# Optimization experiments

Hardware: AMD Instinct MI355X
Metric: run time of the kernel (lower is better)

The kernel has to match this reference:

```python
import jax, jax.numpy as jnp
import numpy as np

N_NODES = 100000
N_EDGES = 1600000
IN_CH = 128


def _sage_conv(x, src, dst, Wl, b, Wr, n_nodes):
    # PyG SAGEConv (aggr='mean', root_weight=True):
    #   out_i = lin_l(mean_{j->i} x_j) + lin_r(x_i)
    msg = x[src]                                             # [E, F]
    agg = jax.ops.segment_sum(msg, dst, num_segments=n_nodes)  # [N, F]
    deg = jax.ops.segment_sum(jnp.ones((src.shape[0],), x.dtype), dst,
                              num_segments=n_nodes)          # [N]
    mean = agg / jnp.maximum(deg, 1.0)[:, None]
    return mean @ Wl + b + x @ Wr


def setup_inputs() -> dict:
    key = jax.random.key(0)
    ks = jax.random.split(key, 10)
    x = jax.random.normal(ks[0], (N_NODES, IN_CH), dtype=jnp.float32)
    edge_index = jax.random.randint(ks[1], (2, N_EDGES), 0, N_NODES, dtype=jnp.int64)
    s = 0.05
    return {
        "x": x,
        "edge_index": edge_index,
        "W1l": jax.random.normal(ks[2], (IN_CH, 32), dtype=jnp.float32) * s,
        "b1": jax.random.normal(ks[3], (32,), dtype=jnp.float32) * s,
        "W1r": jax.random.normal(ks[4], (IN_CH, 32), dtype=jnp.float32) * s,
        "W2l": jax.random.normal(ks[5], (32, 16), dtype=jnp.float32) * s,
        "b2": jax.random.normal(ks[6], (16,), dtype=jnp.float32) * s,
        "W2r": jax.random.normal(ks[7], (32, 16), dtype=jnp.float32) * s,
        "Wfc": jax.random.normal(ks[8], (16, 2), dtype=jnp.float32) * s,
        "bfc": jax.random.normal(ks[9], (2,), dtype=jnp.float32) * s,
    }


def reference(x, edge_index, W1l, b1, W1r, W2l, b2, W2r, Wfc, bfc):
    src, dst = edge_index[0], edge_index[1]
    n = x.shape[0]
    h = jax.nn.relu(_sage_conv(x, src, dst, W1l, b1, W1r, n))   # [N, 32]
    h = jax.nn.relu(_sage_conv(h, src, dst, W2l, b2, W2r, n))   # [N, 16]
    return h @ Wfc + bfc                                        # [N, 2]
```

## Files before the change

kernel.cpp:

```cpp
#include <hip/hip_runtime.h>

#define TPB 256
#define BK_SHIFT 7
#define BK_SIZE 128
#define NBK_MAX 784
#define CAP 2816
#define SC_EPB 8192
#define GEMM_BLKS 1024

typedef __attribute__((ext_vector_type(8))) short bf16x8;
typedef __attribute__((ext_vector_type(4))) float f32x4;
typedef __attribute__((ext_vector_type(2))) float f32x2;
typedef __attribute__((ext_vector_type(4))) unsigned short u16x4;

__device__ __forceinline__ unsigned short f2bf(float f) {
    unsigned u = __float_as_uint(f);
    unsigned r = (u + 0x7FFFu + ((u >> 16) & 1u)) >> 16;
    return (unsigned short)r;
}
__device__ __forceinline__ float bf2f(unsigned short b) {
    return __uint_as_float((unsigned)b << 16);
}
__device__ __forceinline__ void acc4(f32x4& a, u16x4 v) {
    a.x += bf2f(v.x); a.y += bf2f(v.y); a.z += bf2f(v.z); a.w += bf2f(v.w);
}

__global__ __launch_bounds__(256) void build_and_gemm1(
    const int* __restrict__ src, const int* __restrict__ dst,
    int* __restrict__ gfill, int* __restrict__ pk, int E, int NBK, int NSC,
    const float* __restrict__ A,
    const float* __restrict__ Wl,
    const float* __restrict__ Wr,
    const float* __restrict__ b,
    unsigned short* __restrict__ Yb,
    float* __restrict__ C,
    int N)
{
    __shared__ int lcnt[NBK_MAX];
    __shared__ int lbase[NBK_MAX];
    __shared__ int lrank[NBK_MAX];

    if ((int)blockIdx.x < NSC) {
        const int t = threadIdx.x;
        const int e0 = blockIdx.x * SC_EPB;

        for (int i = t; i < NBK; i += 256) { lcnt[i] = 0; lrank[i] = 0; }
        __syncthreads();

        #pragma unroll
        for (int k = 0; k < SC_EPB / 1024; ++k) {
            int e = e0 + k * 1024 + t * 4;
            if (e < E) {
                int4 d = *(const int4*)&dst[e];
                atomicAdd(&lcnt[d.x >> BK_SHIFT], 1);
                atomicAdd(&lcnt[d.y >> BK_SHIFT], 1);
                atomicAdd(&lcnt[d.z >> BK_SHIFT], 1);
                atomicAdd(&lcnt[d.w >> BK_SHIFT], 1);
            }
        }
        __syncthreads();

        for (int i = t; i < NBK; i += 256) {
            int c = lcnt[i];
            if (c) lbase[i] = atomicAdd(&gfill[i], c);
        }
        __syncthreads();

        #pragma unroll
        for (int k = 0; k < SC_EPB / 1024; ++k) {
            int e = e0 + k * 1024 + t * 4;
            if (e < E) {
                int4 d = *(const int4*)&dst[e];
                int4 s = *(const int4*)&src[e];
                {
                    int bb = d.x >> BK_SHIFT;
                    int pos = lbase[bb] + atomicAdd(&lrank[bb], 1);
                    if (pos < CAP) pk[(size_t)bb * CAP + pos] =
                        (s.x << BK_SHIFT) | (d.x & (BK_SIZE - 1));
                }
                {
                    int bb = d.y >> BK_SHIFT;
                    int pos = lbase[bb] + atomicAdd(&lrank[bb], 1);
                    if (pos < CAP) pk[(size_t)bb * CAP + pos] =
                        (s.y << BK_SHIFT) | (d.y & (BK_SIZE - 1));
                }
                {
                    int bb = d.z >> BK_SHIFT;
                    int pos = lbase[bb] + atomicAdd(&lrank[bb], 1);
                    if (pos < CAP) pk[(size_t)bb * CAP + pos] =
                        (s.z << BK_SHIFT) | (d.z & (BK_SIZE - 1));
                }
                {
                    int bb = d.w >> BK_SHIFT;
                    int pos = lbase[bb] + atomicAdd(&lrank[bb], 1);
                    if (pos < CAP) pk[(size_t)bb * CAP + pos] =
                        (s.w << BK_SHIFT) | (d.w & (BK_SIZE - 1));
                }
            }
        }
        return;
    }

    const int lane = threadIdx.x & 63;
    const int m    = lane & 15;
    const int quad = lane >> 4;
    const int wave   = (blockIdx.x - NSC) * (blockDim.x >> 6) + (threadIdx.x >> 6);
    const int nwaves = GEMM_BLKS * (blockDim.x >> 6);
    const int ntiles = (N + 15) >> 4;

    bf16x8 Bf[4][4];
    #pragma unroll
    for (int kc = 0; kc < 4; ++kc) {
        #pragma unroll
        for (int jt = 0; jt < 4; ++jt) {
            const float* W = (jt < 2) ? Wl : Wr;
            const int col = (jt & 1) * 16 + m;
            #pragma unroll
            for (int j = 0; j < 8; ++j) {
                int k = kc * 32 + quad * 8 + j;
                Bf[kc][jt][j] = (short)f2bf(W[k * 32 + col]);
            }
        }
    }

    const float bias0 = b[m];
    const float bias1 = b[16 + m];

    for (int tile = wave; tile < ntiles; tile += nwaves) {
        const int node0 = tile * 16;
        const int gn = node0 + m;
        const bool okA = gn < N;
        const float* rowp = A + (size_t)gn * 128;

        bf16x8 Af[4];
        #pragma unroll
        for (int kc = 0; kc < 4; ++kc) {
            f32x4 v0 = {0.f, 0.f, 0.f, 0.f};
            f32x4 v1 = {0.f, 0.f, 0.f, 0.f};
            if (okA) {
                v0 = __builtin_nontemporal_load((const f32x4*)&rowp[kc * 32 + quad * 8]);
                v1 = __builtin_nontemporal_load((const f32x4*)&rowp[kc * 32 + quad * 8 + 4]);
            }
            Af[kc][0] = (short)f2bf(v0.x); Af[kc][1] = (short)f2bf(v0.y);
            Af[kc][2] = (short)f2bf(v0.z); Af[kc][3] = (short)f2bf(v0.w);
            Af[kc][4] = (short)f2bf(v1.x); Af[kc][5] = (short)f2bf(v1.y);
            Af[kc][6] = (short)f2bf(v1.z); Af[kc][7] = (short)f2bf(v1.w);
        }

        f32x4 acc[4] = {{0.f,0.f,0.f,0.f},{0.f,0.f,0.f,0.f},
                        {0.f,0.f,0.f,0.f},{0.f,0.f,0.f,0.f}};
        #pragma unroll
        for (int kc = 0; kc < 4; ++kc) {
            #pragma unroll
            for (int jt = 0; jt < 4; ++jt)
                acc[jt] = __builtin_amdgcn_mfma_f32_16x16x32_bf16(
                    Af[kc], Bf[kc][jt], acc[jt], 0, 0, 0);
        }

        const int nodeBase = node0 + quad * 4;
        #pragma unroll
        for (int reg = 0; reg < 4; ++reg) {
            const int node = nodeBase + reg;
            if (node < N) {
                Yb[(size_t)node * 32 + m]      = f2bf(acc[0][reg]);
                Yb[(size_t)node * 32 + 16 + m] = f2bf(acc[1][reg]);
                C [(size_t)node * 32 + m]      = acc[2][reg] + bias0;
                C [(size_t)node * 32 + 16 + m] = acc[3][reg] + bias1;
            }
        }
    }
}

__global__ __launch_bounds__(256) void gather_gemm2(
    const int* __restrict__ gfill, const int* __restrict__ pk,
    const unsigned short* __restrict__ Yb,
    const float* __restrict__ c1,
    const float* __restrict__ W2l, const float* __restrict__ W2r,
    const float* __restrict__ b2,
    unsigned short* __restrict__ y2b, float* __restrict__ c2, int N)
{
    __shared__ int lcnt[BK_SIZE];
    __shared__ int soff[BK_SIZE];
    __shared__ int wcur[BK_SIZE];
    __shared__ int sidx[CAP];

    const int t = threadIdx.x;
    const int b = blockIdx.x;
    const size_t base = (size_t)b * CAP;
    const int cnt  = min(gfill[b], CAP);
    const int node0 = b * BK_SIZE;

    if (t < BK_SIZE) lcnt[t] = 0;
    __syncthreads();

    for (int j = t; j < cnt; j += 256)
        atomicAdd(&lcnt[pk[base + j] & (BK_SIZE - 1)], 1);
    __syncthreads();

    int v = (t < BK_SIZE) ? lcnt[t] : 0;
    if (t < BK_SIZE) soff[t] = v;
    __syncthreads();
    for (int off = 1; off < BK_SIZE; off <<= 1) {
        int u = (t < BK_SIZE && t >= off) ? soff[t - off] : 0;
        __syncthreads();
        if (t < BK_SIZE) soff[t] += u;
        __syncthreads();
    }
    if (t < BK_SIZE) wcur[t] = soff[t] - v;
    __syncthreads();

    for (int j = t; j < cnt; j += 256) {
        int pv = pk[base + j];
        int d  = pv & (BK_SIZE - 1);
        int pos = atomicAdd(&wcur[d], 1);
        sidx[pos] = pv >> BK_SHIFT;
    }
    __syncthreads();

    const int q = t & 7;
    #pragma unroll
    for (int pass = 0; pass < 4; ++pass) {
        const int nl = pass * 32 + (t >> 3);
        const int node = node0 + nl;
        const bool active = node < N;
        float h[4] = {0.f, 0.f, 0.f, 0.f};
        if (active) {
            const int deg = lcnt[nl];
            const int en  = soff[nl];
            const int st  = en - deg;
            const float w = 1.0f / fmaxf((float)deg, 1.0f);

            f32x4 a0 = {0.f,0.f,0.f,0.f};
            f32x4 a1 = {0.f,0.f,0.f,0.f};
            f32x4 a2 = {0.f,0.f,0.f,0.f};
            f32x4 a3 = {0.f,0.f,0.f,0.f};
            int j = st;
            for (; j + 3 < en; j += 4) {
                int s0 = sidx[j], s1 = sidx[j+1], s2 = sidx[j+2], s3 = sidx[j+3];
                u16x4 v0 = *(const u16x4*)&Yb[(size_t)s0 * 32 + q * 4];
                u16x4 v1 = *(const u16x4*)&Yb[(size_t)s1 * 32 + q * 4];
                u16x4 v2 = *(const u16x4*)&Yb[(size_t)s2 * 32 + q * 4];
                u16x4 v3 = *(const u16x4*)&Yb[(size_t)s3 * 32 + q * 4];
                acc4(a0, v0); acc4(a1, v1); acc4(a2, v2); acc4(a3, v3);
            }
            for (; j < en; ++j) {
                u16x4 vv = *(const u16x4*)&Yb[(size_t)sidx[j] * 32 + q * 4];
                acc4(a0, vv);
            }
            f32x4 acc;
            acc.x = (a0.x + a1.x) + (a2.x + a3.x);
            acc.y = (a0.y + a1.y) + (a2.y + a3.y);
            acc.z = (a0.z + a1.z) + (a2.z + a3.z);
            acc.w = (a0.w + a1.w) + (a2.w + a3.w);

            f32x4 c = __builtin_nontemporal_load((const f32x4*)&c1[(size_t)node * 32 + q * 4]);
            h[0] = fmaxf(c.x + acc.x * w, 0.f);
            h[1] = fmaxf(c.y + acc.y * w, 0.f);
            h[2] = fmaxf(c.z + acc.z * w, 0.f);
            h[3] = fmaxf(c.w + acc.w * w, 0.f);
        }

        const int  j0  = q * 4;
        const bool isY = (j0 < 16);
        const int  jj  = isY ? j0 : (j0 - 16);
        const float* Wb = isY ? W2l : W2r;

        float o0 = 0.f, o1 = 0.f, o2 = 0.f, o3 = 0.f;
        #pragma unroll
        for (int k = 0; k < 32; ++k) {
            float hk = __shfl(h[k & 3], k >> 2, 8);
            f32x4 wv = *(const f32x4*)&Wb[k * 16 + jj];
            o0 += hk * wv.x; o1 += hk * wv.y; o2 += hk * wv.z; o3 += hk * wv.w;
        }

        if (active) {
            if (isY) {
                u16x4 r;
                r.x = f2bf(o0); r.y = f2bf(o1); r.z = f2bf(o2); r.w = f2bf(o3);
                *(u16x4*)&y2b[(size_t)node * 16 + jj] = r;
            } else {
                f32x4 bb = *(const f32x4*)&b2[jj];
                f32x4 ov = {o0 + bb.x, o1 + bb.y, o2 + bb.z, o3 + bb.w};
                __builtin_nontemporal_store(ov, (f32x4*)&c2[(size_t)node * 16 + jj]);
            }
        }
    }
}

__global__ __launch_bounds__(256) void gather_final(
    const int* __restrict__ gfill, const int* __restrict__ pk,
    const unsigned short* __restrict__ Yb,
    const float* __restrict__ c2,
    const float* __restrict__ Wfc,
    const float* __restrict__ bfc,
    float* __restrict__ out, int N)
{
    __shared__ int lcnt[BK_SIZE];
    __shared__ int soff[BK_SIZE];
    __shared__ int wcur[BK_SIZE];
    __shared__ int sidx[CAP];

    const int t = threadIdx.x;
    const int b = blockIdx.x;
    const size_t base = (size_t)b * CAP;
    const int cnt  = min(gfill[b], CAP);
    const int node0 = b * BK_SIZE;

    if (t < BK_SIZE) lcnt[t] = 0;
    __syncthreads();

    for (int j = t; j < cnt; j += 256)
        atomicAdd(&lcnt[pk[base + j] & (BK_SIZE - 1)], 1);
    __syncthreads();

    int v = (t < BK_SIZE) ? lcnt[t] : 0;
    if (t < BK_SIZE) soff[t] = v;
    __syncthreads();
    for (int off = 1; off < BK_SIZE; off <<= 1) {
        int u = (t < BK_SIZE && t >= off) ? soff[t - off] : 0;
        __syncthreads();
        if (t < BK_SIZE) soff[t] += u;
        __syncthreads();
    }
    if (t < BK_SIZE) wcur[t] = soff[t] - v;
    __syncthreads();

    for (int j = t; j < cnt; j += 256) {
        int pv = pk[base + j];
        int d  = pv & (BK_SIZE - 1);
        int pos = atomicAdd(&wcur[d], 1);
        sidx[pos] = pv >> BK_SHIFT;
    }
    __syncthreads();

    const int q = t & 3;
    #pragma unroll
    for (int pass = 0; pass < 2; ++pass) {
        const int nl = pass * 64 + (t >> 2);
        const int node = node0 + nl;
        if (node < N) {
            const int deg = lcnt[nl];
            const int en  = soff[nl];
            const int st  = en - deg;
            const float w = 1.0f / fmaxf((float)deg, 1.0f);

            f32x4 a0 = {0.f,0.f,0.f,0.f};
            f32x4 a1 = {0.f,0.f,0.f,0.f};
            f32x4 a2 = {0.f,0.f,0.f,0.f};
            f32x4 a3 = {0.f,0.f,0.f,0.f};
            int j = st;
            for (; j + 3 < en; j += 4) {
                int s0 = sidx[j], s1 = sidx[j+1], s2 = sidx[j+2], s3 = sidx[j+3];
                u16x4 v0 = *(const u16x4*)&Yb[(size_t)s0 * 16 + q * 4];
                u16x4 v1 = *(const u16x4*)&Yb[(size_t)s1 * 16 + q * 4];
                u16x4 v2 = *(const u16x4*)&Yb[(size_t)s2 * 16 + q * 4];
                u16x4 v3 = *(const u16x4*)&Yb[(size_t)s3 * 16 + q * 4];
                acc4(a0, v0); acc4(a1, v1); acc4(a2, v2); acc4(a3, v3);
            }
            for (; j < en; ++j) {
                u16x4 vv = *(const u16x4*)&Yb[(size_t)sidx[j] * 16 + q * 4];
                acc4(a0, vv);
            }
            f32x4 acc;
            acc.x = (a0.x + a1.x) + (a2.x + a3.x);
            acc.y = (a0.y + a1.y) + (a2.y + a3.y);
            acc.z = (a0.z + a1.z) + (a2.z + a3.z);
            acc.w = (a0.w + a1.w) + (a2.w + a3.w);

            f32x4 c = __builtin_nontemporal_load((const f32x4*)&c2[(size_t)node * 16 + q * 4]);
            float h0 = fmaxf(c.x + acc.x * w, 0.f);
            float h1 = fmaxf(c.y + acc.y * w, 0.f);
            float h2 = fmaxf(c.z + acc.z * w, 0.f);
            float h3 = fmaxf(c.w + acc.w * w, 0.f);

            const float* Wq = &Wfc[q * 8];
            float o0 = h0 * Wq[0] + h1 * Wq[2] + h2 * Wq[4] + h3 * Wq[6];
            float o1 = h0 * Wq[1] + h1 * Wq[3] + h2 * Wq[5] + h3 * Wq[7];

            o0 += __shfl_xor(o0, 1); o0 += __shfl_xor(o0, 2);
            o1 += __shfl_xor(o1, 1); o1 += __shfl_xor(o1, 2);

            if (q == 0) {
                f32x2 ov = {o0 + bfc[0], o1 + bfc[1]};
                __builtin_nontemporal_store(ov, (f32x2*)&out[(size_t)node * 2]);
            }
        } else {
            float z = 0.f;
            z += __shfl_xor(z, 1); z += __shfl_xor(z, 2);
        }
    }
}

extern "C" void kernel_launch(void* const* d_in, const int* in_sizes, int n_in,
                              void* d_out, int out_size, void* d_ws, size_t ws_size,
                              hipStream_t stream)
{
    const float* x   = (const float*)d_in[0];
    const int*   ei  = (const int*)d_in[1];
    const float* W1l = (const float*)d_in[2];
    const float* b1  = (const float*)d_in[3];
    const float* W1r = (const float*)d_in[4];
    const float* W2l = (const float*)d_in[5];
    const float* b2  = (const float*)d_in[6];
    const float* W2r = (const float*)d_in[7];
    const float* Wfc = (const float*)d_in[8];
    const float* bfc = (const float*)d_in[9];
    float* out = (float*)d_out;

    const int N = in_sizes[0] / 128;
    const int E = in_sizes[1] / 2;
    const int* src = ei;
    const int* dst = ei + E;

    const int NBK = (N + BK_SIZE - 1) / BK_SIZE;
    const int NSC = (E + SC_EPB - 1) / SC_EPB;

    int*   gfill = (int*)d_ws;
    int*   pk    = gfill + NBK_MAX;
    unsigned short* y1b = (unsigned short*)(pk + (size_t)NBK_MAX * CAP);
    float* c1          = (float*)(y1b + (size_t)N * 32);
    unsigned short* y2b = (unsigned short*)(c1 + (size_t)N * 32);
    float* c2          = (float*)(y2b + (size_t)N * 16);

    hipMemsetAsync(gfill, 0, (size_t)NBK_MAX * sizeof(int), stream);
    build_and_gemm1<<<NSC + GEMM_BLKS, TPB, 0, stream>>>(
        src, dst, gfill, pk, E, NBK, NSC,
        x, W1l, W1r, b1, y1b, c1, N);

    gather_gemm2<<<NBK, TPB, 0, stream>>>(
        gfill, pk, y1b, c1, W2l, W2r, b2, y2b, c2, N);

    gather_final<<<NBK, TPB, 0, stream>>>(
        gfill, pk, y2b, c2, Wfc, bfc, out, N);
}
```

Before: 201.9 us.

## Stage bucketed edges in shared memory before coalesced global scatter

The edge-bucketing blocks now run a block-wide prefix scan over per-bucket counts. Each edge is placed into a shared-memory staging buffer sorted by bucket, and the buffer is then written to the global bucket arrays in contiguous runs, replacing scattered per-edge global stores. This adds about 48KB of shared memory to the fused kernel, a 10-step scan with barriers, and an extra pass, and the larger shared footprint may lower occupancy for the GEMM blocks that share this kernel. The other edits are cosmetic reshuffles of the gather loop and a small workspace padding change.

```diff
diff --git a/kernel.cpp b/kernel.cpp
--- a/kernel.cpp
+++ b/kernel.cpp
@@ -36,15 +36,19 @@
     float* __restrict__ C,
     int N)
 {
-    __shared__ int lcnt[NBK_MAX];
+    __shared__ int lcnt [NBK_MAX];
+    __shared__ int soff [1024];
     __shared__ int lbase[NBK_MAX];
     __shared__ int lrank[NBK_MAX];
+    __shared__ int spv  [SC_EPB];
+    __shared__ unsigned short sbk[SC_EPB];
+
+    const int t = threadIdx.x;
 
     if ((int)blockIdx.x < NSC) {
-        const int t = threadIdx.x;
         const int e0 = blockIdx.x * SC_EPB;
 
-        for (int i = t; i < NBK; i += 256) { lcnt[i] = 0; lrank[i] = 0; }
+        for (int i = t; i < NBK_MAX; i += 256) { lcnt[i] = 0; lrank[i] = 0; }
         __syncthreads();
 
         #pragma unroll
@@ -60,6 +64,19 @@
         }
         __syncthreads();
 
+        for (int i = t; i < 1024; i += 256) soff[i] = (i < NBK) ? lcnt[i] : 0;
+        __syncthreads();
+        for (int off = 1; off < 1024; off <<= 1) {
+            int u0 = (t       >= off) ? soff[t       - off] : 0;
+            int u1 = (t + 256 >= off) ? soff[t + 256 - off] : 0;
+            int u2 = (t + 512 >= off) ? soff[t + 512 - off] : 0;
+            int u3 = (t + 768 >= off) ? soff[t + 768 - off] : 0;
+            __syncthreads();
+            soff[t] += u0; soff[t + 256] += u1;
+            soff[t + 512] += u2; soff[t + 768] += u3;
+            __syncthreads();
+        }
+
         for (int i = t; i < NBK; i += 256) {
             int c = lcnt[i];
             if (c) lbase[i] = atomicAdd(&gfill[i], c);
@@ -74,37 +91,45 @@
                 int4 s = *(const int4*)&src[e];
                 {
                     int bb = d.x >> BK_SHIFT;
-                    int pos = lbase[bb] + atomicAdd(&lrank[bb], 1);
-                    if (pos < CAP) pk[(size_t)bb * CAP + pos] =
-                        (s.x << BK_SHIFT) | (d.x & (BK_SIZE - 1));
+                    int pos = (soff[bb] - lcnt[bb]) + atomicAdd(&lrank[bb], 1);
+                    spv[pos] = (s.x << BK_SHIFT) | (d.x & (BK_SIZE - 1));
+                    sbk[pos] = (unsigned short)bb;
                 }
                 {
                     int bb = d.y >> BK_SHIFT;
-                    int pos = lbase[bb] + atomicAdd(&lrank[bb], 1);
-                    if (pos < CAP) pk[(size_t)bb * CAP + pos] =
-                        (s.y << BK_SHIFT) | (d.y & (BK_SIZE - 1));
+                    int pos = (soff[bb] - lcnt[bb]) + atomicAdd(&lrank[bb], 1);
+                    spv[pos] = (s.y << BK_SHIFT) | (d.y & (BK_SIZE - 1));
+                    sbk[pos] = (unsigned short)bb;
                 }
                 {
                     int bb = d.z >> BK_SHIFT;
-                    int pos = lbase[bb] + atomicAdd(&lrank[bb], 1);
-                    if (pos < CAP) pk[(size_t)bb * CAP + pos] =
-                        (s.z << BK_SHIFT) | (d.z & (BK_SIZE - 1));
+                    int pos = (soff[bb] - lcnt[bb]) + atomicAdd(&lrank[bb], 1);
+                    spv[pos] = (s.z << BK_SHIFT) | (d.z & (BK_SIZE - 1));
+                    sbk[pos] = (unsigned short)bb;
                 }
                 {
                     int bb = d.w >> BK_SHIFT;
-                    int pos = lbase[bb] + atomicAdd(&lrank[bb], 1);
-                    if (pos < CAP) pk[(size_t)bb * CAP + pos] =
-                        (s.w << BK_SHIFT) | (d.w & (BK_SIZE - 1));
+                    int pos = (soff[bb] - lcnt[bb]) + atomicAdd(&lrank[bb], 1);
+                    spv[pos] = (s.w << BK_SHIFT) | (d.w & (BK_SIZE - 1));
+                    sbk[pos] = (unsigned short)bb;
                 }
             }
         }
+        __syncthreads();
+
+        const int blockcnt = soff[NBK - 1];
+        for (int i = t; i < blockcnt; i += 256) {
+            int bb = sbk[i];
+            int gpos = lbase[bb] + (i - (soff[bb] - lcnt[bb]));
+            if (gpos < CAP) pk[(size_t)bb * CAP + gpos] = spv[i];
+        }
         return;
     }
 
-    const int lane = threadIdx.x & 63;
+    const int lane = t & 63;
     const int m    = lane & 15;
     const int quad = lane >> 4;
-    const int wave   = (blockIdx.x - NSC) * (blockDim.x >> 6) + (threadIdx.x >> 6);
+    const int wave   = (blockIdx.x - NSC) * (blockDim.x >> 6) + (t >> 6);
     const int nwaves = GEMM_BLKS * (blockDim.x >> 6);
     const int ntiles = (N + 15) >> 4;
 
@@ -351,16 +376,13 @@
             int j = st;
             for (; j + 3 < en; j += 4) {
                 int s0 = sidx[j], s1 = sidx[j+1], s2 = sidx[j+2], s3 = sidx[j+3];
-                u16x4 v0 = *(const u16x4*)&Yb[(size_t)s0 * 16 + q * 4];
-                u16x4 v1 = *(const u16x4*)&Yb[(size_t)s1 * 16 + q * 4];
-                u16x4 v2 = *(const u16x4*)&Yb[(size_t)s2 * 16 + q * 4];
-                u16x4 v3 = *(const u16x4*)&Yb[(size_t)s3 * 16 + q * 4];
-                acc4(a0, v0); acc4(a1, v1); acc4(a2, v2); acc4(a3, v3);
-            }
-            for (; j < en; ++j) {
-                u16x4 vv = *(const u16x4*)&Yb[(size_t)sidx[j] * 16 + q * 4];
-                acc4(a0, vv);
-            }
+                acc4(a0, *(const u16x4*)&Yb[(size_t)s0 * 16 + q * 4]);
+                acc4(a1, *(const u16x4*)&Yb[(size_t)s1 * 16 + q * 4]);
+                acc4(a2, *(const u16x4*)&Yb[(size_t)s2 * 16 + q * 4]);
+                acc4(a3, *(const u16x4*)&Yb[(size_t)s3 * 16 + q * 4]);
+            }
+            for (; j < en; ++j)
+                acc4(a0, *(const u16x4*)&Yb[(size_t)sidx[j] * 16 + q * 4]);
             f32x4 acc;
             acc.x = (a0.x + a1.x) + (a2.x + a3.x);
             acc.y = (a0.y + a1.y) + (a2.y + a3.y);
@@ -416,13 +438,14 @@
     const int NSC = (E + SC_EPB - 1) / SC_EPB;
 
     int*   gfill = (int*)d_ws;
-    int*   pk    = gfill + NBK_MAX;
+    int*   pk    = gfill + NBK_MAX + 16;
     unsigned short* y1b = (unsigned short*)(pk + (size_t)NBK_MAX * CAP);
     float* c1          = (float*)(y1b + (size_t)N * 32);
     unsigned short* y2b = (unsigned short*)(c1 + (size_t)N * 32);
     float* c2          = (float*)(y2b + (size_t)N * 16);
 
-    hipMemsetAsync(gfill, 0, (size_t)NBK_MAX * sizeof(int), stream);
+    hipMemsetAsync(gfill, 0, (size_t)(NBK_MAX + 16) * sizeof(int), stream);
+
     build_and_gemm1<<<NSC + GEMM_BLKS, TPB, 0, stream>>>(
         src, dst, gfill, pk, E, NBK, NSC,
         x, W1l, W1r, b1, y1b, c1, N);
```

Result: faster. 191.4 us (-5.2%).
